# Kernel tuning notes

Hardware: AMD Instinct MI355X
Metric: run time of the kernel (lower is better)

Reference implementation:

```python
import jax, jax.numpy as jnp
import numpy as np

T, B, IN, OUT = 128, 32, 128, 128
N, M, R, H = 256, 64, 4, 256  # mem_slot, mem_size, read_heads, nn_output_size


def setup_inputs() -> dict:
    key = jax.random.key(0)
    ks = jax.random.split(key, 10)
    s = 0.05
    return {
        "xs": jax.random.normal(ks[0], (T, B, IN), jnp.float32),
        "mem0": jax.random.normal(ks[1], (B, N, M), jnp.float32) * s,
        "W_lstm": jax.random.normal(ks[2], (IN + M * R + H, 4 * H), jnp.float32) * s,
        "b_lstm": jnp.zeros((4 * H,), jnp.float32),
        "W_pre": jax.random.normal(ks[3], (H, OUT), jnp.float32) * s,
        "b_pre": jnp.zeros((OUT,), jnp.float32),
        "W_key": jax.random.normal(ks[4], (H, M), jnp.float32) * s,
        "W_beta": jax.random.normal(ks[5], (H, 1), jnp.float32) * s,
        "W_teach": jax.random.normal(ks[6], (H, M), jnp.float32) * s,
        "W_ro": jax.random.normal(ks[7], (M * R, OUT), jnp.float32) * s,
    }


def reference(xs, mem0, W_lstm, b_lstm, W_pre, b_pre, W_key, W_beta, W_teach, W_ro):
    eps = 1e-8

    def step(carry, x):
        mem, h, c, read_vecs, loss = carry
        # controller: LSTM cell over [x, flattened read vectors]
        inp = jnp.concatenate([x, read_vecs.reshape(B, M * R)], axis=-1)
        z = jnp.concatenate([inp, h], axis=-1) @ W_lstm + b_lstm
        i, f, g, o = jnp.split(z, 4, axis=-1)
        c = jax.nn.sigmoid(f) * c + jax.nn.sigmoid(i) * jnp.tanh(g)
        h = jax.nn.sigmoid(o) * jnp.tanh(c)
        pre_out = h @ W_pre + b_pre          # (B, OUT)
        k = h @ W_key                        # (B, M) content key
        beta = jax.nn.softplus(h @ W_beta)   # (B, 1) sharpness
        teacher = h @ W_teach                # (B, M) generated teacher vec
        # cosine similarity between each memory slot and the key
        num = jnp.einsum('bnm,bm->bn', mem, k)
        den = jnp.maximum(
            jnp.linalg.norm(mem, axis=-1) * jnp.linalg.norm(k, axis=-1, keepdims=True), eps)
        sim = num / den                      # (B, N)
        write_w = jax.nn.softmax(beta * sim, axis=-1)  # safe_softmax over slots
        # additive content write (outer product of write weights and key)
        mem = mem + write_w[:, :, None] * k[:, None, :]
        # supervision loss: match generated teacher to written content
        loss = loss + jnp.mean((k - teacher) ** 2)
        # read: write_w broadcast over R heads -> identical reads per head
        read = jnp.einsum('bn,bnm->bm', write_w, mem)  # (B, M)
        read_vecs = jnp.broadcast_to(read[:, :, None], (B, M, R))
        out = pre_out + read_vecs.reshape(B, M * R) @ W_ro
        return (mem, h, c, read_vecs, loss), out

    carry0 = (mem0,
              jnp.zeros((B, H), xs.dtype),
              jnp.zeros((B, H), xs.dtype),
              jnp.zeros((B, M, R), xs.dtype),
              jnp.zeros((), xs.dtype))
    (_, _, _, _, sup_loss), ys = jax.lax.scan(step, carry0, xs)
    return ys, sup_loss
```

## Files before the change

kernel.cpp:

```cpp
#include <hip/hip_runtime.h>

typedef unsigned short u16;
typedef unsigned long long u64;
typedef short short8 __attribute__((ext_vector_type(8)));
typedef float f32x4 __attribute__((ext_vector_type(4)));

__device__ __forceinline__ float b2f(u16 u) {
    unsigned x = ((unsigned)u) << 16;
    return __builtin_bit_cast(float, x);
}
__device__ __forceinline__ u16 f2b(float f) {
    unsigned u = __builtin_bit_cast(unsigned, f);
    u += 0x7FFFu + ((u >> 16) & 1u);
    return (u16)(u >> 16);
}
__device__ __forceinline__ float sigm(float x) { return 1.f / (1.f + __expf(-x)); }
__device__ __forceinline__ float tanh_(float x) { return 1.f - 2.f / (__expf(2.f * x) + 1.f); }

__device__ __forceinline__ uint4 ldg_cv(const void* p) {
    uint4 v;
    asm volatile("global_load_dwordx4 %0, %1, off sc0 sc1\n\ts_waitcnt vmcnt(0)"
                 : "=v"(v) : "v"(p) : "memory");
    return v;
}
__device__ __forceinline__ void ldg_cv4(const void* p0, const void* p1, const void* p2,
                                        const void* p3, uint4& a, uint4& b, uint4& c, uint4& d) {
    asm volatile(
        "global_load_dwordx4 %0, %4, off sc0 sc1\n\t"
        "global_load_dwordx4 %1, %5, off sc0 sc1\n\t"
        "global_load_dwordx4 %2, %6, off sc0 sc1\n\t"
        "global_load_dwordx4 %3, %7, off sc0 sc1\n\t"
        "s_waitcnt vmcnt(0)"
        : "=v"(a), "=v"(b), "=v"(c), "=v"(d)
        : "v"(p0), "v"(p1), "v"(p2), "v"(p3) : "memory");
}
__device__ __forceinline__ void stg_cv(void* p, uint4 v) {
    u64 lo = ((u64)v.y << 32) | (u64)v.x;
    u64 hi = ((u64)v.w << 32) | (u64)v.z;
    __hip_atomic_store((u64*)p,     lo, __ATOMIC_RELAXED, __HIP_MEMORY_SCOPE_AGENT);
    __hip_atomic_store((u64*)p + 1, hi, __ATOMIC_RELAXED, __HIP_MEMORY_SCOPE_AGENT);
}

#define T_STEPS 128
#define BATCH   32
#define KHR     320
#define PADK    328
#define MEMPAD  68
#define WKPAD   264

#define WS_BAR      0
#define WS_LOSS     64
#define WS_FLAG     96
#define WS_HRG      128
#define WS_ZSET     41088
#define WS_XSF      41216
#define WS_MEM0F    2138368
#define WS_WLF      4235520
#define WS_BLF      6856960
#define WS_WPREF    6861056
#define WS_BPREF    6992128
#define WS_WKEYF    6992640
#define WS_WBETAF   7058176
#define WS_WTEACHF  7059200
#define WS_WROF     7124736
#define WS_XW       7255808
#define WS_WREFF    24033024
#define WS_WKT      24295168
#define WS_WROEFF   24360704
#define WS_HS       24393472
#define WS_RS       28587776

#define HR_OFF   0
#define WF_OFF   20992
#define WK_OFF   41472
#define MEM_OFF  75264
#define Z_OFF    144896
#define C_OFF    149504
#define KV_OFF   151552
#define WW_OFF   151808
#define KP_OFF   152832
#define RP_OFF   153856
#define BR_OFF   154880
#define WR_OFF   154944
#define SC_OFF   155008
#define WB_OFF   155072
#define HST_OFF  156096
#define RST_OFF  156608
#define LDS_TOTAL 156736

__device__ __forceinline__ void gridbar(unsigned* bar, unsigned phase) {
    __syncthreads();
    if (threadIdx.x == 0) {
        __builtin_amdgcn_s_waitcnt(0);
        __hip_atomic_fetch_add(bar, 1u, __ATOMIC_RELAXED, __HIP_MEMORY_SCOPE_AGENT);
        const unsigned tgt = phase * 32u;
        long guard = 0;
        while (__hip_atomic_load(bar, __ATOMIC_RELAXED, __HIP_MEMORY_SCOPE_AGENT) < tgt) {
            __builtin_amdgcn_s_sleep(1);
            if (++guard > 3000000L) break;
        }
    }
    __syncthreads();
}

__global__ void dnc_probe(const u16* __restrict__ xs_u16, char* __restrict__ ws) {
    __shared__ int cnt;
    if (threadIdx.x == 0) cnt = 0;
    __syncthreads();
    int c = 0;
    for (int i = threadIdx.x; i < 1024; i += 256) {
        int e = (xs_u16[i] >> 7) & 0xFF;
        if (e >= 96 && e <= 135) c++;
    }
    atomicAdd(&cnt, c);
    __syncthreads();
    if (threadIdx.x == 0) *(int*)(ws + WS_FLAG) = (cnt > 820) ? 1 : 0;
}

__global__ void dnc_normalize(const void* s0, const void* s1, const void* s2, const void* s3,
                              const void* s4, const void* s5, const void* s6, const void* s7,
                              const void* s8, const void* s9, char* __restrict__ ws) {
    const void* srcs[10] = {s0, s1, s2, s3, s4, s5, s6, s7, s8, s9};
    const int sizes[10] = {524288, 524288, 655360, 1024, 32768, 128, 16384, 256, 16384, 32768};
    const int bases[10] = {WS_XSF, WS_MEM0F, WS_WLF, WS_BLF, WS_WPREF, WS_BPREF,
                           WS_WKEYF, WS_WBETAF, WS_WTEACHF, WS_WROF};
    const int bf = *(const int*)(ws + WS_FLAG);
    const int gt = blockIdx.x * 256 + threadIdx.x, gs = gridDim.x * 256;
    for (int s = 0; s < 10; ++s) {
        float* dst = (float*)(ws + bases[s]);
        const int n = sizes[s];
        if (bf) {
            const u16* p = (const u16*)srcs[s];
            for (int i = gt; i < n; i += gs) dst[i] = b2f(p[i]);
        } else {
            const float* p = (const float*)srcs[s];
            for (int i = gt; i < n; i += gs) dst[i] = p[i];
        }
    }
}

__global__ void dnc_prologue(char* __restrict__ ws) {
    extern __shared__ float xls[];
    const float* XSF     = (const float*)(ws + WS_XSF);
    const float* WLF     = (const float*)(ws + WS_WLF);
    const float* BLF     = (const float*)(ws + WS_BLF);
    const float* WKEYF   = (const float*)(ws + WS_WKEYF);
    const float* WTEACHF = (const float*)(ws + WS_WTEACHF);
    const float* WROF    = (const float*)(ws + WS_WROF);
    float* xW  = (float*)(ws + WS_XW);
    float* WrE = (float*)(ws + WS_WREFF);
    float* Wkt = (float*)(ws + WS_WKT);
    float* Wre = (float*)(ws + WS_WROEFF);
    const int wg = blockIdx.x, tid = threadIdx.x;
    if (wg < 256) {
        const int rb = wg >> 3, cb = wg & 7;
        const float4* xsrc = (const float4*)(XSF + (size_t)rb * 16384);
        for (int i = tid; i < 4096; i += 256) {
            float4 v = xsrc[i];
            int row = i >> 5, c4 = (i & 31) * 4;
            float* d = xls + row * 129 + c4;
            d[0] = v.x; d[1] = v.y; d[2] = v.z; d[3] = v.w;
        }
        __syncthreads();
        const int tr = tid >> 4, tc = tid & 15;
        const int c0 = cb * 128 + tc * 8;
        float acc[8][8];
#pragma unroll
        for (int rr = 0; rr < 8; ++rr)
#pragma unroll
            for (int cc = 0; cc < 8; ++cc) acc[rr][cc] = BLF[c0 + cc];
        for (int k = 0; k < 128; ++k) {
            float4 wA = *(const float4*)(WLF + (size_t)k * 1024 + c0);
            float4 wB = *(const float4*)(WLF + (size_t)k * 1024 + c0 + 4);
            float w[8] = {wA.x, wA.y, wA.z, wA.w, wB.x, wB.y, wB.z, wB.w};
#pragma unroll
            for (int rr = 0; rr < 8; ++rr) {
                float xv = xls[(tr * 8 + rr) * 129 + k];
#pragma unroll
                for (int cc = 0; cc < 8; ++cc) acc[rr][cc] += xv * w[cc];
            }
        }
#pragma unroll
        for (int rr = 0; rr < 8; ++rr) {
            size_t o = (size_t)(rb * 128 + tr * 8 + rr) * 1024 + c0;
            *(float4*)(xW + o)     = make_float4(acc[rr][0], acc[rr][1], acc[rr][2], acc[rr][3]);
            *(float4*)(xW + o + 4) = make_float4(acc[rr][4], acc[rr][5], acc[rr][6], acc[rr][7]);
        }
    } else if (wg < 320) {
        const int m = wg - 256;
        const int c = tid * 4;
#pragma unroll
        for (int e = 0; e < 4; ++e) {
            float s = 0.f;
#pragma unroll
            for (int rr = 0; rr < 4; ++rr) s += WLF[(size_t)(128 + 4 * m + rr) * 1024 + c + e];
            WrE[m * 1024 + c + e] = s;
        }
    } else if (wg < 336) {
        const int i = (wg - 320) * 1024 + tid * 4;
#pragma unroll
        for (int e = 0; e < 4; ++e) Wkt[i + e] = WKEYF[i + e] - WTEACHF[i + e];
    } else if (wg < 344) {
        const int i = (wg - 336) * 1024 + tid * 4;
#pragma unroll
        for (int e = 0; e < 4; ++e) {
            int m = (i + e) >> 7, c = (i + e) & 127;
            float s = 0.f;
#pragma unroll
            for (int rr = 0; rr < 4; ++rr) s += WROF[(4 * m + rr) * 128 + c];
            Wre[i + e] = s;
        }
    }
}

__global__ __launch_bounds__(256, 1) void dnc_main(char* __restrict__ ws) {
    extern __shared__ char smem[];
    u16*   hr_lds = (u16*)(smem + HR_OFF);
    u16*   wfrag  = (u16*)(smem + WF_OFF);
    u16*   wkeyT  = (u16*)(smem + WK_OFF);
    float* memA   = (float*)(smem + MEM_OFF);
    float* z_lds  = (float*)(smem + Z_OFF);
    float* c_lds  = (float*)(smem + C_OFF);
    float* kv     = (float*)(smem + KV_OFF);
    float* wwts   = (float*)(smem + WW_OFF);
    float* kpart  = (float*)(smem + KP_OFF);
    float* rp     = (float*)(smem + RP_OFF);
    float* bred   = (float*)(smem + BR_OFF);
    float* wred   = (float*)(smem + WR_OFF);
    float* sc     = (float*)(smem + SC_OFF);
    float* wbF    = (float*)(smem + WB_OFF);
    u16*   hstage = (u16*)(smem + HST_OFF);
    u16*   rstage = (u16*)(smem + RST_OFF);

    const int tid  = threadIdx.x;
    const int wg   = blockIdx.x;
    const int lane = tid & 63;
    const int wid  = tid >> 6;

    unsigned* bar = (unsigned*)(ws + WS_BAR);
    u16* hrg      = (u16*)(ws + WS_HRG);
    const float* xWF     = (const float*)(ws + WS_XW);
    const float* WrEffF  = (const float*)(ws + WS_WREFF);
    const float* WLF     = (const float*)(ws + WS_WLF);
    const float* WKEYF   = (const float*)(ws + WS_WKEYF);
    const float* WBETAF  = (const float*)(ws + WS_WBETAF);
    const float* MEM0F   = (const float*)(ws + WS_MEM0F);
    float* HsF = (float*)(ws + WS_HS);
    float* RsF = (float*)(ws + WS_RS);

    for (int i = tid; i < 32 * PADK; i += 256) hr_lds[i] = 0;
    for (int idx = tid; idx < 10240; idx += 256) {
        int k = idx >> 5, c = idx & 31;
        int kt = k >> 5, q = (k >> 3) & 3, j = k & 7;
        int gcol = (c >> 3) * 256 + wg * 8 + (c & 7);
        float v = (k < 64) ? WrEffF[k * 1024 + gcol]
                           : WLF[(size_t)(384 + (k - 64)) * 1024 + gcol];
        wfrag[((kt * 4 + q) * 32 + c) * 8 + j] = f2b(v);
    }
    for (int i = tid; i < 256 * 64; i += 256) {
        int k = i >> 6, m = i & 63;
        wkeyT[m * WKPAD + k] = f2b(WKEYF[i]);
    }
    wbF[tid]   = WBETAF[tid];
    c_lds[tid] = 0.f;
    for (int i = tid; i < 256 * 64; i += 256) {
        int n = i >> 6, m = i & 63;
        memA[n * MEMPAD + m] = MEM0F[wg * 16384 + i];
    }
    __syncthreads();

    const int bt = wid & 1, ct = wid >> 1;
    const int fm = lane & 15, fq = lane >> 4;
    const int pb = tid >> 3, pu = tid & 7;
    unsigned bar_phase = 0;

    float xg0, xg1, xg2, xg3;
    {
        const size_t xb = (size_t)pb * 1024 + wg * 8 + pu;
        xg0 = xWF[xb]; xg1 = xWF[xb + 256]; xg2 = xWF[xb + 512]; xg3 = xWF[xb + 768];
    }

    for (int t = 0; t < T_STEPS; ++t) {
        {
            uint4 rv = ldg_cv(hrg + pb * KHR + pu * 8);
            *(uint4*)(hr_lds + pb * PADK + pu * 8) = rv;
        }
        __syncthreads();

        f32x4 acc = {0.f, 0.f, 0.f, 0.f};
#pragma unroll
        for (int kt = 0; kt < 10; ++kt) {
            short8 a = *(const short8*)(hr_lds + (bt * 16 + fm) * PADK + kt * 32 + fq * 8);
            short8 b = *(const short8*)(wfrag + ((kt * 4 + fq) * 32 + ct * 16 + fm) * 8);
            acc = __builtin_amdgcn_mfma_f32_16x16x32_bf16(a, b, acc, 0, 0, 0);
        }
#pragma unroll
        for (int r = 0; r < 4; ++r) {
            int bb = bt * 16 + fq * 4 + r;
            int cc = ct * 16 + fm;
            z_lds[bb * 36 + cc] = acc[r];
        }
        __syncthreads();

        {
            float iv = z_lds[pb * 36 + pu]      + xg0;
            float fv = z_lds[pb * 36 + 8 + pu]  + xg1;
            float gv = z_lds[pb * 36 + 16 + pu] + xg2;
            float ov = z_lds[pb * 36 + 24 + pu] + xg3;
            float co = c_lds[pb * 8 + pu];
            float cn = sigm(fv) * co + sigm(iv) * tanh_(gv);
            float hn = sigm(ov) * tanh_(cn);
            c_lds[pb * 8 + pu] = cn;
            hstage[pb * 8 + pu] = f2b(hn);
            HsF[(size_t)(t * BATCH + pb) * 256 + wg * 8 + pu] = hn;
        }
        __syncthreads();
        if (tid < 32) {
            uint4 hv = *(const uint4*)(hstage + tid * 8);
            stg_cv(hrg + tid * KHR + 64 + wg * 8, hv);
        }
        gridbar(bar, ++bar_phase);

        {
            const u16* src = hrg + pb * KHR + 64 + pu * 32;
            uint4 a, b, c, d;
            ldg_cv4(src, src + 8, src + 16, src + 24, a, b, c, d);
            u16* dst = hr_lds + pb * PADK + 64 + pu * 32;
            *(uint4*)(dst)      = a;
            *(uint4*)(dst + 8)  = b;
            *(uint4*)(dst + 16) = c;
            *(uint4*)(dst + 24) = d;
        }
        {
            int tn = (t + 1 < T_STEPS) ? t + 1 : 127;
            const size_t xb = (size_t)(tn * BATCH + pb) * 1024 + wg * 8 + pu;
            xg0 = xWF[xb]; xg1 = xWF[xb + 256]; xg2 = xWF[xb + 512]; xg3 = xWF[xb + 768];
        }
        __syncthreads();

        const u16* hrow = hr_lds + wg * PADK + 64;
        {
            float a = 0.f;
#pragma unroll
            for (int i = 0; i < 8; ++i) {
                short8 w8 = *(const short8*)(wkeyT + lane * WKPAD + wid * 64 + i * 8);
                short8 h8 = *(const short8*)(hrow + wid * 64 + i * 8);
#pragma unroll
                for (int e = 0; e < 8; ++e)
                    a += b2f((u16)h8[e]) * b2f((u16)w8[e]);
            }
            kpart[wid * 64 + lane] = a;
        }
        {
            float bp = b2f(hrow[tid]) * wbF[tid];
#pragma unroll
            for (int off = 32; off > 0; off >>= 1) bp += __shfl_xor(bp, off, 64);
            if (lane == 0) bred[wid] = bp;
        }
        __syncthreads();
        if (tid < 64) {
            float kk = kpart[tid] + kpart[64 + tid] + kpart[128 + tid] + kpart[192 + tid];
            kv[tid] = kk;
            float k2 = kk * kk;
#pragma unroll
            for (int off = 32; off > 0; off >>= 1) k2 += __shfl_xor(k2, off, 64);
            if (tid == 0) sc[1] = sqrtf(k2);
        } else if (tid == 64) {
            float zb = bred[0] + bred[1] + bred[2] + bred[3];
            sc[0] = logf(1.f + __expf(zb));
        }
        __syncthreads();
        const float beta = sc[0], knorm = sc[1];

        float num = 0.f, nr2 = 0.f;
        {
            const float4* mrow = (const float4*)(memA + tid * MEMPAD);
            const float4* k4p  = (const float4*)kv;
#pragma unroll
            for (int i = 0; i < 16; ++i) {
                float4 m4 = mrow[i], k4 = k4p[i];
                num += m4.x * k4.x + m4.y * k4.y + m4.z * k4.z + m4.w * k4.w;
                nr2 += m4.x * m4.x + m4.y * m4.y + m4.z * m4.z + m4.w * m4.w;
            }
        }
        float den = fmaxf(sqrtf(nr2) * knorm, 1e-8f);
        float s   = beta * (num / den);
        float wm = s;
#pragma unroll
        for (int off = 32; off > 0; off >>= 1) wm = fmaxf(wm, __shfl_xor(wm, off, 64));
        float ev = __expf(s - wm);
        float wsum = ev;
#pragma unroll
        for (int off = 32; off > 0; off >>= 1) wsum += __shfl_xor(wsum, off, 64);
        if (lane == 0) { wred[wid] = wm; wred[8 + wid] = wsum; }
        __syncthreads();
        float gm = fmaxf(fmaxf(wred[0], wred[1]), fmaxf(wred[2], wred[3]));
        float gs = wred[8]  * __expf(wred[0] - gm) + wred[9]  * __expf(wred[1] - gm)
                 + wred[10] * __expf(wred[2] - gm) + wred[11] * __expf(wred[3] - gm);
        float w = __expf(s - gm) / gs;
        wwts[tid] = w;
        __syncthreads();

        {
            const int lm = lane & 15, q = lane >> 4;
            float4 k4 = ((const float4*)kv)[lm];
            float r0 = 0.f, r1 = 0.f, r2 = 0.f, r3 = 0.f;
#pragma unroll
            for (int i = 0; i < 16; ++i) {
                int n = wid * 64 + i * 4 + q;
                float wn = wwts[n];
                float4* mp = (float4*)(memA + n * MEMPAD + 4 * lm);
                float4 m4 = *mp;
                m4.x += wn * k4.x; m4.y += wn * k4.y; m4.z += wn * k4.z; m4.w += wn * k4.w;
                *mp = m4;
                r0 += wn * m4.x; r1 += wn * m4.y; r2 += wn * m4.z; r3 += wn * m4.w;
            }
            r0 += __shfl_xor(r0, 16, 64); r0 += __shfl_xor(r0, 32, 64);
            r1 += __shfl_xor(r1, 16, 64); r1 += __shfl_xor(r1, 32, 64);
            r2 += __shfl_xor(r2, 16, 64); r2 += __shfl_xor(r2, 32, 64);
            r3 += __shfl_xor(r3, 16, 64); r3 += __shfl_xor(r3, 32, 64);
            if (q == 0) {
                rp[wid * 64 + 4 * lm + 0] = r0;
                rp[wid * 64 + 4 * lm + 1] = r1;
                rp[wid * 64 + 4 * lm + 2] = r2;
                rp[wid * 64 + 4 * lm + 3] = r3;
            }
        }
        __syncthreads();
        if (tid < 64) {
            float rd = rp[tid] + rp[64 + tid] + rp[128 + tid] + rp[192 + tid];
            rstage[tid] = f2b(rd);
            RsF[(size_t)(t * BATCH + wg) * 64 + tid] = rd;
        }
        __syncthreads();
        if (tid < 8) {
            uint4 rv = *(const uint4*)(rstage + tid * 8);
            stg_cv(hrg + wg * KHR + tid * 8, rv);
        }
        gridbar(bar, ++bar_phase);
    }
}

__global__ void dnc_epilogue(char* __restrict__ ws, void* __restrict__ outv) {
    __shared__ float hs8[8][256];
    __shared__ float rs8[8][64];
    __shared__ float lacc;
    const float* HsF   = (const float*)(ws + WS_HS);
    const float* RsF   = (const float*)(ws + WS_RS);
    const float* WktF  = (const float*)(ws + WS_WKT);
    const float* WreF  = (const float*)(ws + WS_WROEFF);
    const float* WpreF = (const float*)(ws + WS_WPREF);
    const float* bpreF = (const float*)(ws + WS_BPREF);
    float* lossacc = (float*)(ws + WS_LOSS);
    const int bf = *(const int*)(ws + WS_FLAG);
    const int tid = threadIdx.x;
    const size_t r0 = (size_t)blockIdx.x * 8;
    if (tid == 0) lacc = 0.f;
    for (int i = tid; i < 8 * 256; i += 256) hs8[i >> 8][i & 255] = HsF[r0 * 256 + i];
    for (int i = tid; i < 8 * 64; i += 256)  rs8[i >> 6][i & 63]  = RsF[r0 * 64 + i];
    __syncthreads();
    {
        const int rl = tid >> 5, c0 = (tid & 31) * 4;
        float a0 = bpreF[c0], a1 = bpreF[c0 + 1], a2 = bpreF[c0 + 2], a3 = bpreF[c0 + 3];
        for (int k = 0; k < 256; ++k) {
            float hv = hs8[rl][k];
            float4 w4 = *(const float4*)(WpreF + k * 128 + c0);
            a0 += hv * w4.x; a1 += hv * w4.y; a2 += hv * w4.z; a3 += hv * w4.w;
        }
        for (int m = 0; m < 64; ++m) {
            float rv = rs8[rl][m];
            float4 w4 = *(const float4*)(WreF + m * 128 + c0);
            a0 += rv * w4.x; a1 += rv * w4.y; a2 += rv * w4.z; a3 += rv * w4.w;
        }
        size_t o = (r0 + rl) * 128 + c0;
        if (bf) {
            u16* out = (u16*)outv;
            out[o] = f2b(a0); out[o + 1] = f2b(a1); out[o + 2] = f2b(a2); out[o + 3] = f2b(a3);
        } else {
            float* out = (float*)outv;
            out[o] = a0; out[o + 1] = a1; out[o + 2] = a2; out[o + 3] = a3;
        }
    }
    {
        const int rl = tid >> 5, m0 = (tid & 31) * 2;
        float d0 = 0.f, d1 = 0.f;
        for (int k = 0; k < 256; ++k) {
            float hv = hs8[rl][k];
            d0 += hv * WktF[k * 64 + m0];
            d1 += hv * WktF[k * 64 + m0 + 1];
        }
        float p = d0 * d0 + d1 * d1;
#pragma unroll
        for (int off = 32; off > 0; off >>= 1) p += __shfl_xor(p, off, 64);
        if ((tid & 63) == 0) atomicAdd(&lacc, p);
        __syncthreads();
        if (tid == 0) atomicAdd(lossacc, lacc);
    }
}

__global__ void dnc_loss_fin(const char* __restrict__ ws, void* __restrict__ outv) {
    if (threadIdx.x == 0 && blockIdx.x == 0) {
        float l = *(const float*)(ws + WS_LOSS) * (1.f / 2048.f);
        if (*(const int*)(ws + WS_FLAG)) ((u16*)outv)[524288] = f2b(l);
        else                             ((float*)outv)[524288] = l;
    }
}

extern "C" void kernel_launch(void* const* d_in, const int* in_sizes, int n_in,
                              void* d_out, int out_size, void* d_ws, size_t ws_size,
                              hipStream_t stream) {
    char* ws = (char*)d_ws;
    hipMemsetAsync(d_ws, 0, WS_ZSET, stream);
    dnc_probe<<<1, 256, 0, stream>>>((const u16*)d_in[0], ws);
    dnc_normalize<<<512, 256, 0, stream>>>(d_in[0], d_in[1], d_in[2], d_in[3], d_in[4],
                                           d_in[5], d_in[6], d_in[7], d_in[8], d_in[9], ws);
    (void)hipFuncSetAttribute((const void*)dnc_prologue,
                              hipFuncAttributeMaxDynamicSharedMemorySize, 128 * 129 * 4);
    dnc_prologue<<<344, 256, 128 * 129 * 4, stream>>>(ws);
    (void)hipFuncSetAttribute((const void*)dnc_main,
                              hipFuncAttributeMaxDynamicSharedMemorySize, LDS_TOTAL);
    dnc_main<<<32, 256, LDS_TOTAL, stream>>>(ws);
    dnc_epilogue<<<512, 256, 0, stream>>>(ws, d_out);
    dnc_loss_fin<<<1, 64, 0, stream>>>(ws, d_out);
}
```

Baseline: 1.243 ms.

## Use per-block flag grid barrier and precompute h-part of LSTM GEMM early

Replaces the single atomic-counter grid barrier with per-block phase flags that one wavefront polls with a ballot, removing contention on one counter. It splits the gate GEMM so the h-dependent k-tiles are computed right after h arrives and carried into the next step, leaving only the read-vector tiles on the critical path after the second barrier. It also overlaps the h reload with the memory row-norm computation by deferring the load wait. The flag barrier drops the explicit waitcnt before signalling and relies on relaxed stores for ordering, which adds some risk.

```diff
diff --git a/kernel.cpp b/kernel.cpp
--- a/kernel.cpp
+++ b/kernel.cpp
@@ -23,16 +23,18 @@
                  : "=v"(v) : "v"(p) : "memory");
     return v;
 }
-__device__ __forceinline__ void ldg_cv4(const void* p0, const void* p1, const void* p2,
-                                        const void* p3, uint4& a, uint4& b, uint4& c, uint4& d) {
+__device__ __forceinline__ void ldg_cv4_issue(const void* p0, const void* p1, const void* p2,
+                                              const void* p3, uint4& a, uint4& b, uint4& c, uint4& d) {
     asm volatile(
         "global_load_dwordx4 %0, %4, off sc0 sc1\n\t"
         "global_load_dwordx4 %1, %5, off sc0 sc1\n\t"
         "global_load_dwordx4 %2, %6, off sc0 sc1\n\t"
-        "global_load_dwordx4 %3, %7, off sc0 sc1\n\t"
-        "s_waitcnt vmcnt(0)"
+        "global_load_dwordx4 %3, %7, off sc0 sc1"
         : "=v"(a), "=v"(b), "=v"(c), "=v"(d)
         : "v"(p0), "v"(p1), "v"(p2), "v"(p3) : "memory");
+}
+__device__ __forceinline__ void wait_vm0() {
+    asm volatile("s_waitcnt vmcnt(0)" ::: "memory");
 }
 __device__ __forceinline__ void stg_cv(void* p, uint4 v) {
     u64 lo = ((u64)v.y << 32) | (u64)v.x;
@@ -49,9 +51,9 @@
 #define WKPAD   264
 
 #define WS_BAR      0
-#define WS_LOSS     64
-#define WS_FLAG     96
-#define WS_HRG      128
+#define WS_LOSS     128
+#define WS_FLAG     160
+#define WS_HRG      192
 #define WS_ZSET     41088
 #define WS_XSF      41216
 #define WS_MEM0F    2138368
@@ -88,16 +90,19 @@
 #define RST_OFF  156608
 #define LDS_TOTAL 156736
 
-__device__ __forceinline__ void gridbar(unsigned* bar, unsigned phase) {
+__device__ __forceinline__ void gridbar(unsigned* flags, unsigned phase) {
     __syncthreads();
-    if (threadIdx.x == 0) {
-        __builtin_amdgcn_s_waitcnt(0);
-        __hip_atomic_fetch_add(bar, 1u, __ATOMIC_RELAXED, __HIP_MEMORY_SCOPE_AGENT);
-        const unsigned tgt = phase * 32u;
+    if (threadIdx.x < 64) {
+        if (threadIdx.x == 0)
+            __hip_atomic_store(flags + blockIdx.x, phase, __ATOMIC_RELAXED,
+                               __HIP_MEMORY_SCOPE_AGENT);
         long guard = 0;
-        while (__hip_atomic_load(bar, __ATOMIC_RELAXED, __HIP_MEMORY_SCOPE_AGENT) < tgt) {
+        for (;;) {
+            unsigned v = __hip_atomic_load(flags + (threadIdx.x & 31), __ATOMIC_RELAXED,
+                                           __HIP_MEMORY_SCOPE_AGENT);
+            if (__ballot(v < phase) == 0ull) break;
+            if (++guard > 2000000L) break;
             __builtin_amdgcn_s_sleep(1);
-            if (++guard > 3000000L) break;
         }
     }
     __syncthreads();
@@ -237,8 +242,8 @@
     const int lane = tid & 63;
     const int wid  = tid >> 6;
 
-    unsigned* bar = (unsigned*)(ws + WS_BAR);
-    u16* hrg      = (u16*)(ws + WS_HRG);
+    unsigned* flags = (unsigned*)(ws + WS_BAR);
+    u16* hrg        = (u16*)(ws + WS_HRG);
     const float* xWF     = (const float*)(ws + WS_XW);
     const float* WrEffF  = (const float*)(ws + WS_WREFF);
     const float* WLF     = (const float*)(ws + WS_WLF);
@@ -279,6 +284,7 @@
         const size_t xb = (size_t)pb * 1024 + wg * 8 + pu;
         xg0 = xWF[xb]; xg1 = xWF[xb + 256]; xg2 = xWF[xb + 512]; xg3 = xWF[xb + 768];
     }
+    f32x4 hWacc = {0.f, 0.f, 0.f, 0.f};
 
     for (int t = 0; t < T_STEPS; ++t) {
         {
@@ -287,9 +293,9 @@
         }
         __syncthreads();
 
-        f32x4 acc = {0.f, 0.f, 0.f, 0.f};
-#pragma unroll
-        for (int kt = 0; kt < 10; ++kt) {
+        f32x4 acc = hWacc;
+#pragma unroll
+        for (int kt = 0; kt < 2; ++kt) {
             short8 a = *(const short8*)(hr_lds + (bt * 16 + fm) * PADK + kt * 32 + fq * 8);
             short8 b = *(const short8*)(wfrag + ((kt * 4 + fq) * 32 + ct * 16 + fm) * 8);
             acc = __builtin_amdgcn_mfma_f32_16x16x32_bf16(a, b, acc, 0, 0, 0);
@@ -319,24 +325,47 @@
             uint4 hv = *(const uint4*)(hstage + tid * 8);
             stg_cv(hrg + tid * KHR + 64 + wg * 8, hv);
         }
-        gridbar(bar, ++bar_phase);
-
+        gridbar(flags, ++bar_phase);
+
+        uint4 ha, hb4, hc, hd;
         {
             const u16* src = hrg + pb * KHR + 64 + pu * 32;
-            uint4 a, b, c, d;
-            ldg_cv4(src, src + 8, src + 16, src + 24, a, b, c, d);
-            u16* dst = hr_lds + pb * PADK + 64 + pu * 32;
-            *(uint4*)(dst)      = a;
-            *(uint4*)(dst + 8)  = b;
-            *(uint4*)(dst + 16) = c;
-            *(uint4*)(dst + 24) = d;
+            ldg_cv4_issue(src, src + 8, src + 16, src + 24, ha, hb4, hc, hd);
         }
         {
             int tn = (t + 1 < T_STEPS) ? t + 1 : 127;
             const size_t xb = (size_t)(tn * BATCH + pb) * 1024 + wg * 8 + pu;
             xg0 = xWF[xb]; xg1 = xWF[xb + 256]; xg2 = xWF[xb + 512]; xg3 = xWF[xb + 768];
         }
-        __syncthreads();
+        float nr2 = 0.f;
+        {
+            const float4* mrow = (const float4*)(memA + tid * MEMPAD);
+#pragma unroll
+            for (int i = 0; i < 16; ++i) {
+                float4 m4 = mrow[i];
+                nr2 += m4.x * m4.x + m4.y * m4.y + m4.z * m4.z + m4.w * m4.w;
+            }
+        }
+        wait_vm0();
+        {
+            u16* dst = hr_lds + pb * PADK + 64 + pu * 32;
+            *(uint4*)(dst)      = ha;
+            *(uint4*)(dst + 8)  = hb4;
+            *(uint4*)(dst + 16) = hc;
+            *(uint4*)(dst + 24) = hd;
+        }
+        __syncthreads();
+
+        {
+            f32x4 hz = {0.f, 0.f, 0.f, 0.f};
+#pragma unroll
+            for (int kt = 2; kt < 10; ++kt) {
+                short8 a = *(const short8*)(hr_lds + (bt * 16 + fm) * PADK + kt * 32 + fq * 8);
+                short8 b = *(const short8*)(wfrag + ((kt * 4 + fq) * 32 + ct * 16 + fm) * 8);
+                hz = __builtin_amdgcn_mfma_f32_16x16x32_bf16(a, b, hz, 0, 0, 0);
+            }
+            hWacc = hz;
+        }
 
         const u16* hrow = hr_lds + wg * PADK + 64;
         {
@@ -372,7 +401,7 @@
         __syncthreads();
         const float beta = sc[0], knorm = sc[1];
 
-        float num = 0.f, nr2 = 0.f;
+        float num = 0.f;
         {
             const float4* mrow = (const float4*)(memA + tid * MEMPAD);
             const float4* k4p  = (const float4*)kv;
@@ -380,7 +409,6 @@
             for (int i = 0; i < 16; ++i) {
                 float4 m4 = mrow[i], k4 = k4p[i];
                 num += m4.x * k4.x + m4.y * k4.y + m4.z * k4.z + m4.w * k4.w;
-                nr2 += m4.x * m4.x + m4.y * m4.y + m4.z * m4.z + m4.w * m4.w;
             }
         }
         float den = fmaxf(sqrtf(nr2) * knorm, 1e-8f);
@@ -395,9 +423,9 @@
         if (lane == 0) { wred[wid] = wm; wred[8 + wid] = wsum; }
         __syncthreads();
         float gm = fmaxf(fmaxf(wred[0], wred[1]), fmaxf(wred[2], wred[3]));
-        float gs = wred[8]  * __expf(wred[0] - gm) + wred[9]  * __expf(wred[1] - gm)
-                 + wred[10] * __expf(wred[2] - gm) + wred[11] * __expf(wred[3] - gm);
-        float w = __expf(s - gm) / gs;
+        float gsum = wred[8]  * __expf(wred[0] - gm) + wred[9]  * __expf(wred[1] - gm)
+                   + wred[10] * __expf(wred[2] - gm) + wred[11] * __expf(wred[3] - gm);
+        float w = __expf(s - gm) / gsum;
         wwts[tid] = w;
         __syncthreads();
 
@@ -437,7 +465,7 @@
             uint4 rv = *(const uint4*)(rstage + tid * 8);
             stg_cv(hrg + wg * KHR + tid * 8, rv);
         }
-        gridbar(bar, ++bar_phase);
+        gridbar(flags, ++bar_phase);
     }
 }
 
```

Result: faster. 1.163 ms (-6.4%).

## Replace grid-barrier column-split LSTM with per-batch blocks holding weights in registers

Applied to the files above, without the earlier changes.

The recurrent kernel no longer splits LSTM gate columns across 32 workgroups with global exchange and two grid barriers per step. Each workgroup now owns one batch element and computes the full 1024-wide gate GEMV with scalar FMAs. It uses bf16-packed weights, 128 rows kept in registers and the remaining 192 rows streamed from global each step. A new pack kernel precomputes the packed read-summed weights. This removes the cross-block synchronisation latency, but each block now does 32x more GEMV work without MFMA, and it adds register pressure and per-step global weight traffic.

```diff
diff --git a/kernel.cpp b/kernel.cpp
--- a/kernel.cpp
+++ b/kernel.cpp
@@ -3,7 +3,6 @@
 typedef unsigned short u16;
 typedef unsigned long long u64;
 typedef short short8 __attribute__((ext_vector_type(8)));
-typedef float f32x4 __attribute__((ext_vector_type(4)));
 
 __device__ __forceinline__ float b2f(u16 u) {
     unsigned x = ((unsigned)u) << 16;
@@ -14,46 +13,27 @@
     u += 0x7FFFu + ((u >> 16) & 1u);
     return (u16)(u >> 16);
 }
+__device__ __forceinline__ float lo16(unsigned u) {
+    return __builtin_bit_cast(float, u << 16);
+}
+__device__ __forceinline__ float hi16(unsigned u) {
+    return __builtin_bit_cast(float, u & 0xFFFF0000u);
+}
 __device__ __forceinline__ float sigm(float x) { return 1.f / (1.f + __expf(-x)); }
 __device__ __forceinline__ float tanh_(float x) { return 1.f - 2.f / (__expf(2.f * x) + 1.f); }
 
-__device__ __forceinline__ uint4 ldg_cv(const void* p) {
-    uint4 v;
-    asm volatile("global_load_dwordx4 %0, %1, off sc0 sc1\n\ts_waitcnt vmcnt(0)"
-                 : "=v"(v) : "v"(p) : "memory");
-    return v;
-}
-__device__ __forceinline__ void ldg_cv4(const void* p0, const void* p1, const void* p2,
-                                        const void* p3, uint4& a, uint4& b, uint4& c, uint4& d) {
-    asm volatile(
-        "global_load_dwordx4 %0, %4, off sc0 sc1\n\t"
-        "global_load_dwordx4 %1, %5, off sc0 sc1\n\t"
-        "global_load_dwordx4 %2, %6, off sc0 sc1\n\t"
-        "global_load_dwordx4 %3, %7, off sc0 sc1\n\t"
-        "s_waitcnt vmcnt(0)"
-        : "=v"(a), "=v"(b), "=v"(c), "=v"(d)
-        : "v"(p0), "v"(p1), "v"(p2), "v"(p3) : "memory");
-}
-__device__ __forceinline__ void stg_cv(void* p, uint4 v) {
-    u64 lo = ((u64)v.y << 32) | (u64)v.x;
-    u64 hi = ((u64)v.w << 32) | (u64)v.z;
-    __hip_atomic_store((u64*)p,     lo, __ATOMIC_RELAXED, __HIP_MEMORY_SCOPE_AGENT);
-    __hip_atomic_store((u64*)p + 1, hi, __ATOMIC_RELAXED, __HIP_MEMORY_SCOPE_AGENT);
-}
-
 #define T_STEPS 128
 #define BATCH   32
-#define KHR     320
-#define PADK    328
 #define MEMPAD  68
 #define WKPAD   264
-
-#define WS_BAR      0
-#define WS_LOSS     64
-#define WS_FLAG     96
-#define WS_HRG      128
+#define KREG    128
+#define KTOT    320
+
+#define WS_LOSS     128
+#define WS_FLAG     160
 #define WS_ZSET     41088
 #define WS_XSF      41216
+#define WS_WPK      41216
 #define WS_MEM0F    2138368
 #define WS_WLF      4235520
 #define WS_BLF      6856960
@@ -64,44 +44,24 @@
 #define WS_WTEACHF  7059200
 #define WS_WROF     7124736
 #define WS_XW       7255808
-#define WS_WREFF    24033024
 #define WS_WKT      24295168
 #define WS_WROEFF   24360704
 #define WS_HS       24393472
 #define WS_RS       28587776
 
-#define HR_OFF   0
-#define WF_OFF   20992
-#define WK_OFF   41472
-#define MEM_OFF  75264
-#define Z_OFF    144896
-#define C_OFF    149504
-#define KV_OFF   151552
-#define WW_OFF   151808
-#define KP_OFF   152832
-#define RP_OFF   153856
-#define BR_OFF   154880
-#define WR_OFF   154944
-#define SC_OFF   155008
-#define WB_OFF   155072
-#define HST_OFF  156096
-#define RST_OFF  156608
-#define LDS_TOTAL 156736
-
-__device__ __forceinline__ void gridbar(unsigned* bar, unsigned phase) {
-    __syncthreads();
-    if (threadIdx.x == 0) {
-        __builtin_amdgcn_s_waitcnt(0);
-        __hip_atomic_fetch_add(bar, 1u, __ATOMIC_RELAXED, __HIP_MEMORY_SCOPE_AGENT);
-        const unsigned tgt = phase * 32u;
-        long guard = 0;
-        while (__hip_atomic_load(bar, __ATOMIC_RELAXED, __HIP_MEMORY_SCOPE_AGENT) < tgt) {
-            __builtin_amdgcn_s_sleep(1);
-            if (++guard > 3000000L) break;
-        }
-    }
-    __syncthreads();
-}
+#define MEM_OFF  0
+#define WK_OFF   69632
+#define Z_OFF    103424
+#define HRF_OFF  107520
+#define HBB_OFF  108800
+#define WB_OFF   109312
+#define KV_OFF   110336
+#define WW_OFF   110592
+#define KP_OFF   111616
+#define RP_OFF   112640
+#define WR_OFF   113664
+#define SC_OFF   113728
+#define LDS_TOTAL 113792
 
 __global__ void dnc_probe(const u16* __restrict__ xs_u16, char* __restrict__ ws) {
     __shared__ int cnt;
@@ -148,7 +108,6 @@
     const float* WTEACHF = (const float*)(ws + WS_WTEACHF);
     const float* WROF    = (const float*)(ws + WS_WROF);
     float* xW  = (float*)(ws + WS_XW);
-    float* WrE = (float*)(ws + WS_WREFF);
     float* Wkt = (float*)(ws + WS_WKT);
     float* Wre = (float*)(ws + WS_WROEFF);
     const int wg = blockIdx.x, tid = threadIdx.x;
@@ -186,22 +145,12 @@
             *(float4*)(xW + o)     = make_float4(acc[rr][0], acc[rr][1], acc[rr][2], acc[rr][3]);
             *(float4*)(xW + o + 4) = make_float4(acc[rr][4], acc[rr][5], acc[rr][6], acc[rr][7]);
         }
-    } else if (wg < 320) {
-        const int m = wg - 256;
-        const int c = tid * 4;
-#pragma unroll
-        for (int e = 0; e < 4; ++e) {
-            float s = 0.f;
-#pragma unroll
-            for (int rr = 0; rr < 4; ++rr) s += WLF[(size_t)(128 + 4 * m + rr) * 1024 + c + e];
-            WrE[m * 1024 + c + e] = s;
-        }
-    } else if (wg < 336) {
-        const int i = (wg - 320) * 1024 + tid * 4;
+    } else if (wg < 272) {
+        const int i = (wg - 256) * 1024 + tid * 4;
 #pragma unroll
         for (int e = 0; e < 4; ++e) Wkt[i + e] = WKEYF[i + e] - WTEACHF[i + e];
-    } else if (wg < 344) {
-        const int i = (wg - 336) * 1024 + tid * 4;
+    } else if (wg < 280) {
+        const int i = (wg - 272) * 1024 + tid * 4;
 #pragma unroll
         for (int e = 0; e < 4; ++e) {
             int m = (i + e) >> 7, c = (i + e) & 127;
@@ -213,138 +162,134 @@
     }
 }
 
+__global__ void dnc_pack(char* __restrict__ ws) {
+    const float* WLF = (const float*)(ws + WS_WLF);
+    unsigned* Wpk = (unsigned*)(ws + WS_WPK);
+    const int k = blockIdx.x, tid = threadIdx.x;
+#pragma unroll
+    for (int j = 0; j < 2; ++j) {
+        int c2 = tid * 2 + j;
+        float lo, hi;
+        if (k < 64) {
+            lo = 0.f; hi = 0.f;
+#pragma unroll
+            for (int rr = 0; rr < 4; ++rr) {
+                const float* row = WLF + (size_t)(128 + 4 * k + rr) * 1024;
+                lo += row[2 * c2]; hi += row[2 * c2 + 1];
+            }
+        } else {
+            const float* row = WLF + (size_t)(384 + k - 64) * 1024;
+            lo = row[2 * c2]; hi = row[2 * c2 + 1];
+        }
+        Wpk[k * 512 + c2] = ((unsigned)f2b(hi) << 16) | (unsigned)f2b(lo);
+    }
+}
+
 __global__ __launch_bounds__(256, 1) void dnc_main(char* __restrict__ ws) {
     extern __shared__ char smem[];
-    u16*   hr_lds = (u16*)(smem + HR_OFF);
-    u16*   wfrag  = (u16*)(smem + WF_OFF);
-    u16*   wkeyT  = (u16*)(smem + WK_OFF);
-    float* memA   = (float*)(smem + MEM_OFF);
-    float* z_lds  = (float*)(smem + Z_OFF);
-    float* c_lds  = (float*)(smem + C_OFF);
-    float* kv     = (float*)(smem + KV_OFF);
-    float* wwts   = (float*)(smem + WW_OFF);
-    float* kpart  = (float*)(smem + KP_OFF);
-    float* rp     = (float*)(smem + RP_OFF);
-    float* bred   = (float*)(smem + BR_OFF);
-    float* wred   = (float*)(smem + WR_OFF);
-    float* sc     = (float*)(smem + SC_OFF);
-    float* wbF    = (float*)(smem + WB_OFF);
-    u16*   hstage = (u16*)(smem + HST_OFF);
-    u16*   rstage = (u16*)(smem + RST_OFF);
+    float* memA = (float*)(smem + MEM_OFF);
+    u16*  wkeyT = (u16*)(smem + WK_OFF);
+    float* z_lds = (float*)(smem + Z_OFF);
+    float* hrF  = (float*)(smem + HRF_OFF);
+    u16*  hbB   = (u16*)(smem + HBB_OFF);
+    float* wbF  = (float*)(smem + WB_OFF);
+    float* kv   = (float*)(smem + KV_OFF);
+    float* wwts = (float*)(smem + WW_OFF);
+    float* kpart = (float*)(smem + KP_OFF);
+    float* rp   = (float*)(smem + RP_OFF);
+    float* wred = (float*)(smem + WR_OFF);
+    float* sc   = (float*)(smem + SC_OFF);
 
     const int tid  = threadIdx.x;
-    const int wg   = blockIdx.x;
+    const int b    = blockIdx.x;
     const int lane = tid & 63;
     const int wid  = tid >> 6;
 
-    unsigned* bar = (unsigned*)(ws + WS_BAR);
-    u16* hrg      = (u16*)(ws + WS_HRG);
-    const float* xWF     = (const float*)(ws + WS_XW);
-    const float* WrEffF  = (const float*)(ws + WS_WREFF);
-    const float* WLF     = (const float*)(ws + WS_WLF);
-    const float* WKEYF   = (const float*)(ws + WS_WKEYF);
-    const float* WBETAF  = (const float*)(ws + WS_WBETAF);
-    const float* MEM0F   = (const float*)(ws + WS_MEM0F);
+    const unsigned* Wpk = (const unsigned*)(ws + WS_WPK);
+    const uint2* Wpk2   = (const uint2*)Wpk;
+    const float* xWF    = (const float*)(ws + WS_XW);
+    const float* WKEYF  = (const float*)(ws + WS_WKEYF);
+    const float* WBETAF = (const float*)(ws + WS_WBETAF);
+    const float* MEM0F  = (const float*)(ws + WS_MEM0F);
     float* HsF = (float*)(ws + WS_HS);
     float* RsF = (float*)(ws + WS_RS);
 
-    for (int i = tid; i < 32 * PADK; i += 256) hr_lds[i] = 0;
-    for (int idx = tid; idx < 10240; idx += 256) {
-        int k = idx >> 5, c = idx & 31;
-        int kt = k >> 5, q = (k >> 3) & 3, j = k & 7;
-        int gcol = (c >> 3) * 256 + wg * 8 + (c & 7);
-        float v = (k < 64) ? WrEffF[k * 1024 + gcol]
-                           : WLF[(size_t)(384 + (k - 64)) * 1024 + gcol];
-        wfrag[((kt * 4 + q) * 32 + c) * 8 + j] = f2b(v);
-    }
     for (int i = tid; i < 256 * 64; i += 256) {
         int k = i >> 6, m = i & 63;
         wkeyT[m * WKPAD + k] = f2b(WKEYF[i]);
     }
-    wbF[tid]   = WBETAF[tid];
-    c_lds[tid] = 0.f;
+    wbF[tid] = WBETAF[tid];
+    for (int i = tid; i < 320; i += 256) hrF[i] = 0.f;
     for (int i = tid; i < 256 * 64; i += 256) {
         int n = i >> 6, m = i & 63;
-        memA[n * MEMPAD + m] = MEM0F[wg * 16384 + i];
-    }
+        memA[n * MEMPAD + m] = MEM0F[b * 16384 + i];
+    }
+    uint2 wreg2[KREG];
+#pragma unroll
+    for (int k = 0; k < KREG; ++k) wreg2[k] = Wpk2[k * 256 + tid];
+    float c_reg = 0.f;
     __syncthreads();
 
-    const int bt = wid & 1, ct = wid >> 1;
-    const int fm = lane & 15, fq = lane >> 4;
-    const int pb = tid >> 3, pu = tid & 7;
-    unsigned bar_phase = 0;
-
-    float xg0, xg1, xg2, xg3;
-    {
-        const size_t xb = (size_t)pb * 1024 + wg * 8 + pu;
-        xg0 = xWF[xb]; xg1 = xWF[xb + 256]; xg2 = xWF[xb + 512]; xg3 = xWF[xb + 768];
-    }
-
     for (int t = 0; t < T_STEPS; ++t) {
-        {
-            uint4 rv = ldg_cv(hrg + pb * KHR + pu * 8);
-            *(uint4*)(hr_lds + pb * PADK + pu * 8) = rv;
-        }
-        __syncthreads();
-
-        f32x4 acc = {0.f, 0.f, 0.f, 0.f};
-#pragma unroll
-        for (int kt = 0; kt < 10; ++kt) {
-            short8 a = *(const short8*)(hr_lds + (bt * 16 + fm) * PADK + kt * 32 + fq * 8);
-            short8 b = *(const short8*)(wfrag + ((kt * 4 + fq) * 32 + ct * 16 + fm) * 8);
-            acc = __builtin_amdgcn_mfma_f32_16x16x32_bf16(a, b, acc, 0, 0, 0);
-        }
-#pragma unroll
-        for (int r = 0; r < 4; ++r) {
-            int bb = bt * 16 + fq * 4 + r;
-            int cc = ct * 16 + fm;
-            z_lds[bb * 36 + cc] = acc[r];
-        }
-        __syncthreads();
-
-        {
-            float iv = z_lds[pb * 36 + pu]      + xg0;
-            float fv = z_lds[pb * 36 + 8 + pu]  + xg1;
-            float gv = z_lds[pb * 36 + 16 + pu] + xg2;
-            float ov = z_lds[pb * 36 + 24 + pu] + xg3;
-            float co = c_lds[pb * 8 + pu];
-            float cn = sigm(fv) * co + sigm(iv) * tanh_(gv);
+        const size_t xb = (size_t)(t * BATCH + b) * 1024 + tid;
+        float xg0 = xWF[xb];
+        float xg1 = xWF[xb + 256];
+        float xg2 = xWF[xb + 512];
+        float xg3 = xWF[xb + 768];
+
+        float a0 = 0.f, a1 = 0.f, a2 = 0.f, a3 = 0.f;
+        {
+            const float4* hr4 = (const float4*)hrF;
+#pragma unroll
+            for (int kq = 0; kq < KREG / 4; ++kq) {
+                float4 h4 = hr4[kq];
+                float hh[4] = {h4.x, h4.y, h4.z, h4.w};
+#pragma unroll
+                for (int j = 0; j < 4; ++j) {
+                    uint2 w = wreg2[kq * 4 + j];
+                    float h = hh[j];
+                    a0 += h * lo16(w.x); a1 += h * hi16(w.x);
+                    a2 += h * lo16(w.y); a3 += h * hi16(w.y);
+                }
+            }
+#pragma unroll 1
+            for (int kc = 0; kc < (KTOT - KREG) / 16; ++kc) {
+                uint2 st[16];
+#pragma unroll
+                for (int i = 0; i < 16; ++i)
+                    st[i] = Wpk2[(KREG + kc * 16 + i) * 256 + tid];
+#pragma unroll
+                for (int i = 0; i < 16; ++i) {
+                    float h = hrF[KREG + kc * 16 + i];
+                    uint2 w = st[i];
+                    a0 += h * lo16(w.x); a1 += h * hi16(w.x);
+                    a2 += h * lo16(w.y); a3 += h * hi16(w.y);
+                }
+            }
+        }
+        *(float4*)(z_lds + 4 * tid) = make_float4(a0, a1, a2, a3);
+        __syncthreads();
+
+        {
+            float iv = z_lds[tid]       + xg0;
+            float fv = z_lds[256 + tid] + xg1;
+            float gv = z_lds[512 + tid] + xg2;
+            float ov = z_lds[768 + tid] + xg3;
+            float cn = sigm(fv) * c_reg + sigm(iv) * tanh_(gv);
             float hn = sigm(ov) * tanh_(cn);
-            c_lds[pb * 8 + pu] = cn;
-            hstage[pb * 8 + pu] = f2b(hn);
-            HsF[(size_t)(t * BATCH + pb) * 256 + wg * 8 + pu] = hn;
-        }
-        __syncthreads();
-        if (tid < 32) {
-            uint4 hv = *(const uint4*)(hstage + tid * 8);
-            stg_cv(hrg + tid * KHR + 64 + wg * 8, hv);
-        }
-        gridbar(bar, ++bar_phase);
-
-        {
-            const u16* src = hrg + pb * KHR + 64 + pu * 32;
-            uint4 a, b, c, d;
-            ldg_cv4(src, src + 8, src + 16, src + 24, a, b, c, d);
-            u16* dst = hr_lds + pb * PADK + 64 + pu * 32;
-            *(uint4*)(dst)      = a;
-            *(uint4*)(dst + 8)  = b;
-            *(uint4*)(dst + 16) = c;
-            *(uint4*)(dst + 24) = d;
-        }
-        {
-            int tn = (t + 1 < T_STEPS) ? t + 1 : 127;
-            const size_t xb = (size_t)(tn * BATCH + pb) * 1024 + wg * 8 + pu;
-            xg0 = xWF[xb]; xg1 = xWF[xb + 256]; xg2 = xWF[xb + 512]; xg3 = xWF[xb + 768];
-        }
-        __syncthreads();
-
-        const u16* hrow = hr_lds + wg * PADK + 64;
+            c_reg = cn;
+            hbB[tid] = f2b(hn);
+            hrF[64 + tid] = hn;
+            HsF[(size_t)(t * BATCH + b) * 256 + tid] = hn;
+        }
+        __syncthreads();
+
         {
             float a = 0.f;
 #pragma unroll
             for (int i = 0; i < 8; ++i) {
                 short8 w8 = *(const short8*)(wkeyT + lane * WKPAD + wid * 64 + i * 8);
-                short8 h8 = *(const short8*)(hrow + wid * 64 + i * 8);
+                short8 h8 = *(const short8*)(hbB + wid * 64 + i * 8);
 #pragma unroll
                 for (int e = 0; e < 8; ++e)
                     a += b2f((u16)h8[e]) * b2f((u16)w8[e]);
@@ -352,10 +297,10 @@
             kpart[wid * 64 + lane] = a;
         }
         {
-            float bp = b2f(hrow[tid]) * wbF[tid];
+            float bp = b2f(hbB[tid]) * wbF[tid];
 #pragma unroll
             for (int off = 32; off > 0; off >>= 1) bp += __shfl_xor(bp, off, 64);
-            if (lane == 0) bred[wid] = bp;
+            if (lane == 0) wred[12 + wid] = bp;
         }
         __syncthreads();
         if (tid < 64) {
@@ -366,7 +311,7 @@
             for (int off = 32; off > 0; off >>= 1) k2 += __shfl_xor(k2, off, 64);
             if (tid == 0) sc[1] = sqrtf(k2);
         } else if (tid == 64) {
-            float zb = bred[0] + bred[1] + bred[2] + bred[3];
+            float zb = wred[12] + wred[13] + wred[14] + wred[15];
             sc[0] = logf(1.f + __expf(zb));
         }
         __syncthreads();
@@ -395,9 +340,9 @@
         if (lane == 0) { wred[wid] = wm; wred[8 + wid] = wsum; }
         __syncthreads();
         float gm = fmaxf(fmaxf(wred[0], wred[1]), fmaxf(wred[2], wred[3]));
-        float gs = wred[8]  * __expf(wred[0] - gm) + wred[9]  * __expf(wred[1] - gm)
-                 + wred[10] * __expf(wred[2] - gm) + wred[11] * __expf(wred[3] - gm);
-        float w = __expf(s - gm) / gs;
+        float gsum = wred[8]  * __expf(wred[0] - gm) + wred[9]  * __expf(wred[1] - gm)
+                   + wred[10] * __expf(wred[2] - gm) + wred[11] * __expf(wred[3] - gm);
+        float w = __expf(s - gm) / gsum;
         wwts[tid] = w;
         __syncthreads();
 
@@ -429,15 +374,10 @@
         __syncthreads();
         if (tid < 64) {
             float rd = rp[tid] + rp[64 + tid] + rp[128 + tid] + rp[192 + tid];
-            rstage[tid] = f2b(rd);
-            RsF[(size_t)(t * BATCH + wg) * 64 + tid] = rd;
-        }
-        __syncthreads();
-        if (tid < 8) {
-            uint4 rv = *(const uint4*)(rstage + tid * 8);
-            stg_cv(hrg + wg * KHR + tid * 8, rv);
-        }
-        gridbar(bar, ++bar_phase);
+            hrF[tid] = rd;
+            RsF[(size_t)(t * BATCH + b) * 64 + tid] = rd;
+        }
+        __syncthreads();
     }
 }
 
@@ -516,7 +456,8 @@
                                            d_in[5], d_in[6], d_in[7], d_in[8], d_in[9], ws);
     (void)hipFuncSetAttribute((const void*)dnc_prologue,
                               hipFuncAttributeMaxDynamicSharedMemorySize, 128 * 129 * 4);
-    dnc_prologue<<<344, 256, 128 * 129 * 4, stream>>>(ws);
+    dnc_prologue<<<280, 256, 128 * 129 * 4, stream>>>(ws);
+    dnc_pack<<<320, 256, 0, stream>>>(ws);
     (void)hipFuncSetAttribute((const void*)dnc_main,
                               hipFuncAttributeMaxDynamicSharedMemorySize, LDS_TOTAL);
     dnc_main<<<32, 256, LDS_TOTAL, stream>>>(ws);
```

Measured after the change: 2.287 ms. +84.0%, slower.
